# Kernel tuning notes

Hardware: AMD Instinct MI355X
Metric: run time of the kernel (lower is better)

Reference implementation:

```python
import jax, jax.numpy as jnp
import numpy as np

NUM_SEGMENT = 10
TIME_DURATION = 1.0
DT = TIME_DURATION / NUM_SEGMENT
N2 = 2
NUM_DATA = 2_000_000
HAM_MODEL = jnp.array([[0.0, 0.5], [0.5, 0.0]], dtype=jnp.complex64)  # 0.5 * sigma_x
TARGET_GATE = jnp.array([[0.0, 1.0], [1.0, 0.0]], dtype=jnp.complex64)  # sigma_x


def setup_inputs() -> dict:
    key = jax.random.key(0)
    k1, k2, k3 = jax.random.split(key, 3)
    para_ham_unknown = jax.random.uniform(k1, (N2, N2), jnp.float32, -0.1, 0.1)
    omega_data = jax.random.uniform(k2, (NUM_DATA, NUM_SEGMENT), jnp.float32, -0.1, 0.1)
    infedility_data = jax.random.uniform(k3, (NUM_DATA,), jnp.float32, 0.0, 0.1)
    return {"para_ham_unknown": para_ham_unknown, "omega_data": omega_data,
            "infedility_data": infedility_data}


def _real_matrix_to_hermitian(x):
    # symmetric real part + antisymmetric imaginary part -> Hermitian
    xc = x.astype(jnp.complex64)
    return (xc + xc.T) * 0.5 + 1j * (xc - xc.T) * 0.5


def reference(para_ham_unknown, omega_data, infedility_data):
    eye = jnp.eye(N2, dtype=jnp.complex64)
    herm = _real_matrix_to_hermitian(para_ham_unknown)
    ham_unknown = herm - jnp.trace(herm) * eye / N2  # traceless
    H = HAM_MODEL + ham_unknown                       # (2,2) Hermitian
    tr = jnp.trace(H)                                 # ~0 here, kept for generality
    H0 = H - tr * eye / N2                            # traceless part
    # For traceless 2x2 Hermitian H0: H0 @ H0 = r^2 I
    rsq = (jnp.einsum('ij,ji->', H0, H0).real) / N2
    r = jnp.sqrt(jnp.maximum(rsq, 1e-30))

    def step(unitary, omega_x):
        # closed-form: exp(-1j*phi*H) = e^{-i phi tr/2} (cos(phi r) I - i sin(phi r)/r H0)
        phi = DT * omega_x                            # (B,)
        theta = phi * r
        sinc = jnp.where(rsq > 1e-24, jnp.sin(theta) / r, phi)
        phase = jnp.exp(-1j * phi.astype(jnp.complex64) * tr / 2.0)
        u_step = phase[:, None, None] * (
            jnp.cos(theta).astype(jnp.complex64)[:, None, None] * eye
            - 1j * sinc.astype(jnp.complex64)[:, None, None] * H0)
        return jnp.einsum('bij,bjk->bik', u_step, unitary), None

    B = omega_data.shape[0]
    u0 = jnp.broadcast_to(eye, (B, N2, N2))
    unitary, _ = jax.lax.scan(step, u0, omega_data.T)  # scan over segments

    # tmp0[b] = trace(target_gate^H @ unitary[b])
    tmp0 = jnp.sum(TARGET_GATE.conj()[None, :, :] * unitary, axis=(1, 2))
    infidelity = 1.0 - (tmp0 * tmp0.conj()).real / (N2 * N2)
    loss = jnp.mean((infedility_data - infidelity) ** 2)
    return loss
```

## Files before the change

### kernel.cpp

```cpp
#include <hip/hip_runtime.h>


#define ND 2000000
#define BLK 256
#define ROWS_PER_BLOCK 1024
#define F4_PER_BLOCK 2560
#define NBLOCKS ((ND + ROWS_PER_BLOCK - 1) / ROWS_PER_BLOCK)

__device__ __forceinline__ float sin_small(float th) {
    const float t2 = th * th;
    return th * (1.0f + t2 * (-(1.0f / 6.0f) + t2 * (1.0f / 120.0f)));
}

__global__ __launch_bounds__(256) void loss_kernel(
    const float* __restrict__ para,
    const float* __restrict__ omega,
    const float* __restrict__ infid,
    float* __restrict__ partial) {

    __shared__ float lds[11264];

    const float x00 = para[0], x01 = para[1], x10 = para[2], x11 = para[3];
    const float a  = 0.5f * (x00 - x11);
    const float cr = 0.5f + 0.5f * (x01 + x10);
    const float ci = 0.5f * (x01 - x10);
    const float r  = sqrtf(a * a + cr * cr + ci * ci);
    const float cr_over_r = cr / r;
    const float dt_r = 0.1f * r;

    const unsigned t = threadIdx.x;
    const unsigned base_row  = (unsigned)blockIdx.x * ROWS_PER_BLOCK;
    const unsigned tile_rows = min((unsigned)ROWS_PER_BLOCK, (unsigned)ND - base_row);
    const unsigned nf4       = (tile_rows * 10u) >> 2;

    const float4* gof4 = (const float4*)omega + (size_t)blockIdx.x * F4_PER_BLOCK;
    #pragma unroll
    for (int j = 0; j < 10; ++j) {
        const unsigned m = t + 256u * (unsigned)j;
        if (m < nf4) {
            const float4 v = gof4[m];
            const unsigned pf4 = m + m / 10u;
            *(float4*)&lds[4u * pf4] = v;
        }
    }
    __syncthreads();

    float acc = 0.0f;
    #pragma unroll
    for (int k = 0; k < 4; ++k) {
        const unsigned row = t + 256u * (unsigned)k;
        if (row < tile_rows) {
            const unsigned w = 44u * (row >> 2) + 10u * (row & 3u);
            const float2 a0 = *(const float2*)&lds[w + 0];
            const float2 a1 = *(const float2*)&lds[w + 2];
            const float2 a2 = *(const float2*)&lds[w + 4];
            const float2 a3 = *(const float2*)&lds[w + 6];
            const float2 a4 = *(const float2*)&lds[w + 8];
            const float s = (((a0.x + a0.y) + (a1.x + a1.y))
                          +  ((a2.x + a2.y) + (a3.x + a3.y))) + (a4.x + a4.y);

            const float tq = cr_over_r * sin_small(dt_r * s);
            const float d  = infid[base_row + row] - (1.0f - tq * tq);
            acc += d * d;
        }
    }

    #pragma unroll
    for (int off = 32; off > 0; off >>= 1)
        acc += __shfl_down(acc, off, 64);

    __shared__ float wsum[4];
    const int lane = threadIdx.x & 63;
    const int w    = threadIdx.x >> 6;
    if (lane == 0) wsum[w] = acc;
    __syncthreads();
    if (threadIdx.x == 0) {
        partial[blockIdx.x] = (wsum[0] + wsum[1]) + (wsum[2] + wsum[3]);
    }
}

__global__ __launch_bounds__(256) void reduce_kernel(
    const float* __restrict__ partial,
    float* __restrict__ out) {

    const int tid = threadIdx.x;
    float acc = 0.0f;
    #pragma unroll
    for (int i = 0; i < (NBLOCKS + 255) / 256; ++i) {
        const int idx = tid + 256 * i;
        if (idx < NBLOCKS) acc += partial[idx];
    }

    #pragma unroll
    for (int off = 32; off > 0; off >>= 1)
        acc += __shfl_down(acc, off, 64);

    __shared__ float wsum[4];
    const int lane = tid & 63;
    const int w    = tid >> 6;
    if (lane == 0) wsum[w] = acc;
    __syncthreads();
    if (tid == 0)
        out[0] = ((wsum[0] + wsum[1]) + (wsum[2] + wsum[3])) * (1.0f / (float)ND);
}

extern "C" void kernel_launch(void* const* d_in, const int* in_sizes, int n_in,
                              void* d_out, int out_size, void* d_ws, size_t ws_size,
                              hipStream_t stream) {
    const float* para  = (const float*)d_in[0];
    const float* omega = (const float*)d_in[1];
    const float* infid = (const float*)d_in[2];
    float* out     = (float*)d_out;
    float* partial = (float*)d_ws;

    loss_kernel<<<NBLOCKS, BLK, 0, stream>>>(para, omega, infid, partial);
    reduce_kernel<<<1, 256, 0, stream>>>(partial, out);
}
```

Baseline: 132.2 us.

## Stage omega tiles via direct global-to-LDS loads and prefetch infidelity values

```diff
diff --git a/kernel.cpp b/kernel.cpp
--- a/kernel.cpp
+++ b/kernel.cpp
@@ -4,8 +4,12 @@
 #define ND 2000000
 #define BLK 256
 #define ROWS_PER_BLOCK 1024
-#define F4_PER_BLOCK 2560
+#define TILE_BYTES (ROWS_PER_BLOCK * 40)
+#define NCHUNK (TILE_BYTES / 1024)
 #define NBLOCKS ((ND + ROWS_PER_BLOCK - 1) / ROWS_PER_BLOCK)
+
+typedef __attribute__((address_space(1))) const void gvoid_t;
+typedef __attribute__((address_space(3))) void lvoid_t;
 
 __device__ __forceinline__ float sin_small(float th) {
     const float t2 = th * th;
@@ -18,7 +22,7 @@
     const float* __restrict__ infid,
     float* __restrict__ partial) {
 
-    __shared__ float lds[11264];
+    __shared__ float lds[TILE_BYTES / 4];
 
     const float x00 = para[0], x01 = para[1], x10 = para[2], x11 = para[3];
     const float a  = 0.5f * (x00 - x11);
@@ -28,21 +32,34 @@
     const float cr_over_r = cr / r;
     const float dt_r = 0.1f * r;
 
-    const unsigned t = threadIdx.x;
+    const unsigned t    = threadIdx.x;
+    const unsigned lane = t & 63u;
+    const unsigned wave = t >> 6;
     const unsigned base_row  = (unsigned)blockIdx.x * ROWS_PER_BLOCK;
     const unsigned tile_rows = min((unsigned)ROWS_PER_BLOCK, (unsigned)ND - base_row);
-    const unsigned nf4       = (tile_rows * 10u) >> 2;
+    const unsigned tile_bytes = tile_rows * 40u;
 
-    const float4* gof4 = (const float4*)omega + (size_t)blockIdx.x * F4_PER_BLOCK;
+    const char* gtile = (const char*)omega + (size_t)base_row * 40u;
     #pragma unroll
-    for (int j = 0; j < 10; ++j) {
-        const unsigned m = t + 256u * (unsigned)j;
-        if (m < nf4) {
-            const float4 v = gof4[m];
-            const unsigned pf4 = m + m / 10u;
-            *(float4*)&lds[4u * pf4] = v;
+    for (int j = 0; j < NCHUNK / 4; ++j) {
+        const unsigned c  = wave * (NCHUNK / 4) + (unsigned)j;
+        const unsigned cb = c * 1024u;
+        if (cb + 1024u <= tile_bytes) {
+            __builtin_amdgcn_global_load_lds(
+                (gvoid_t*)(gtile + cb + lane * 16u),
+                (lvoid_t*)((char*)lds + cb),
+                16, 0, 0);
         }
     }
+
+    float fi[4];
+    #pragma unroll
+    for (int k = 0; k < 4; ++k) {
+        const unsigned row = t + 256u * (unsigned)k;
+        fi[k] = (row < tile_rows) ? infid[base_row + row] : 0.0f;
+    }
+
+    asm volatile("s_waitcnt vmcnt(0)" ::: "memory");
     __syncthreads();
 
     float acc = 0.0f;
@@ -50,7 +67,7 @@
     for (int k = 0; k < 4; ++k) {
         const unsigned row = t + 256u * (unsigned)k;
         if (row < tile_rows) {
-            const unsigned w = 44u * (row >> 2) + 10u * (row & 3u);
+            const unsigned w = row * 10u;
             const float2 a0 = *(const float2*)&lds[w + 0];
             const float2 a1 = *(const float2*)&lds[w + 2];
             const float2 a2 = *(const float2*)&lds[w + 4];
@@ -60,7 +77,7 @@
                           +  ((a2.x + a2.y) + (a3.x + a3.y))) + (a4.x + a4.y);
 
             const float tq = cr_over_r * sin_small(dt_r * s);
-            const float d  = infid[base_row + row] - (1.0f - tq * tq);
+            const float d  = fi[k] - (1.0f - tq * tq);
             acc += d * d;
         }
     }
@@ -70,7 +87,6 @@
         acc += __shfl_down(acc, off, 64);
 
     __shared__ float wsum[4];
-    const int lane = threadIdx.x & 63;
     const int w    = threadIdx.x >> 6;
     if (lane == 0) wsum[w] = acc;
     __syncthreads();
```

Result: faster. 123.6 us (-6.5%).
